# Performance work log

Hardware: AMD Instinct MI355X
Metric: run time of the kernel (lower is better)

The kernel has to match this reference:

```python
import jax, jax.numpy as jnp
import numpy as np

N = 2_000_000
NUM_IN = 9
F1, F2 = 32, 64
NUM_SEG = 100_000
EPS = 1e-5


def setup_inputs() -> dict:
    key = jax.random.key(0)
    ks = jax.random.split(key, 10)
    points = jax.random.normal(ks[0], (N, NUM_IN), dtype=jnp.float32)
    inverse_indices = jax.random.randint(ks[1], (N,), 0, NUM_SEG, dtype=jnp.int64)
    w1 = jax.random.normal(ks[2], (NUM_IN, F1), dtype=jnp.float32) / np.sqrt(NUM_IN)
    b1 = jax.random.normal(ks[3], (F1,), dtype=jnp.float32) * 0.01
    g1 = jnp.ones((F1,), jnp.float32)
    be1 = jnp.zeros((F1,), jnp.float32)
    w2 = jax.random.normal(ks[4], (F1, F2), dtype=jnp.float32) / np.sqrt(F1)
    b2 = jax.random.normal(ks[5], (F2,), dtype=jnp.float32) * 0.01
    g2 = jnp.ones((F2,), jnp.float32)
    be2 = jnp.zeros((F2,), jnp.float32)
    return {
        "points": points, "inverse_indices": inverse_indices, "num_segments": NUM_SEG,
        "w1": w1, "b1": b1, "g1": g1, "be1": be1,
        "w2": w2, "b2": b2, "g2": g2, "be2": be2,
    }


def _linear_bn_relu(x, w, b, gamma, beta):
    # Linear -> BatchNorm1d (training-mode batch stats, biased var, eps=1e-5) -> ReLU
    h = x @ w + b
    mean = h.mean(axis=0)
    var = h.var(axis=0)  # biased, matches torch BN normalization
    h = (h - mean) * jax.lax.rsqrt(var + EPS) * gamma + beta
    return jax.nn.relu(h)


def reference(points, inverse_indices, num_segments, w1, b1, g1, be1, w2, b2, g2, be2):
    feat = _linear_bn_relu(points, w1, b1, g1, be1)
    feat = _linear_bn_relu(feat, w2, b2, g2, be2)
    # scatter_max over dim 0; torch_scatter zero-initializes empty segments,
    # and post-ReLU features are >= 0, so clamp -inf (empty) to 0.
    seg = jax.ops.segment_max(feat, inverse_indices, num_segments=num_segments)
    return jnp.maximum(seg, 0.0)
```

## Files before the change

kernel.cpp:

```cpp
#include <hip/hip_runtime.h>

#define EPS 1e-5f
#define NIN 9
#define F1 32
#define F2 64
#define NMOM 45
#define ROWB 80
#define SHIFT 7
#define NSEGB 128
#define NBMAX 1024
#define BT_BIN 8192
#define WSTRIDE 68
#define NREP 16

#define WS_SC1  192
#define WS_SH1  224
#define WS_W1P  256
#define WS_SC2  544
#define WS_SH2  608

typedef __attribute__((ext_vector_type(8))) short bf16x8;
typedef __attribute__((ext_vector_type(4))) float f32x4;

__device__ __forceinline__ unsigned int f2bf(float f) {
    unsigned int u = __float_as_uint(f);
    return (u + 0x7fffu + ((u >> 16) & 1u)) >> 16;
}
__device__ __forceinline__ unsigned int pack2(float lo, float hi) {
    unsigned int r;
    asm("v_cvt_pk_bf16_f32 %0, %1, %2" : "=v"(r) : "v"(lo), "v"(hi));
    return r;
}

__device__ __forceinline__ void load_pt9(const float* __restrict__ p, float* __restrict__ x)
{
    const float4* p4 = (const float4*)p;
    const float4 a = p4[0];
    const float4 b = p4[1];
    x[0] = a.x; x[1] = a.y; x[2] = a.z; x[3] = a.w;
    x[4] = b.x; x[5] = b.y; x[6] = b.z; x[7] = b.w;
    x[8] = p[8];
}

#define FOR_S(OP) OP(0) OP(1) OP(2) OP(3) OP(4) OP(5) OP(6) OP(7) OP(8)
#define FOR_M(OP) \
    OP(0,0) OP(0,1) OP(0,2) OP(0,3) OP(0,4) OP(0,5) OP(0,6) OP(0,7) OP(0,8) \
    OP(1,1) OP(1,2) OP(1,3) OP(1,4) OP(1,5) OP(1,6) OP(1,7) OP(1,8) \
    OP(2,2) OP(2,3) OP(2,4) OP(2,5) OP(2,6) OP(2,7) OP(2,8) \
    OP(3,3) OP(3,4) OP(3,5) OP(3,6) OP(3,7) OP(3,8) \
    OP(4,4) OP(4,5) OP(4,6) OP(4,7) OP(4,8) \
    OP(5,5) OP(5,6) OP(5,7) OP(5,8) \
    OP(6,6) OP(6,7) OP(6,8) \
    OP(7,7) OP(7,8) \
    OP(8,8)
#define MIDX(k,l) ((k)*NIN - ((k)*((k)-1))/2 + ((l)-(k)))
#define S_DECL(k)   float S_##k = 0.f;
#define M_DECL(k,l) float M_##k##_##l = 0.f;
#define S_ACC(k)    S_##k += x[k];
#define M_ACC(k,l)  M_##k##_##l = fmaf(x[k], x[l], M_##k##_##l);
#define S_RED(k)    S_##k += __shfl_xor(S_##k, off, 64);
#define M_RED(k,l)  M_##k##_##l += __shfl_xor(M_##k##_##l, off, 64);
#define S_ATM(k)    atomicAdd(&red[(k)], S_##k);
#define M_ATM(k,l)  atomicAdd(&red[16 + MIDX(k,l)], M_##k##_##l);

__global__ __launch_bounds__(256, 4) void moments_kernel(
    const float* __restrict__ pts, float* __restrict__ wsrep, int N)
{
    __shared__ float red[64];

    FOR_S(S_DECL)
    FOR_M(M_DECL)

    const int stride = gridDim.x * blockDim.x;
    for (int i = blockIdx.x * blockDim.x + threadIdx.x; i < N; i += stride) {
        float x[NIN];
        load_pt9(pts + (size_t)i * NIN, x);
        FOR_S(S_ACC)
        FOR_M(M_ACC)
    }
#pragma unroll
    for (int off = 32; off > 0; off >>= 1) {
        FOR_S(S_RED)
        FOR_M(M_RED)
    }
    if (threadIdx.x < 64) red[threadIdx.x] = 0.f;
    __syncthreads();
    if ((threadIdx.x & 63) == 0) {
        FOR_S(S_ATM)
        FOR_M(M_ATM)
    }
    __syncthreads();
    if (threadIdx.x < 64)
        atomicAdd(&wsrep[(blockIdx.x & (NREP - 1)) * 64 + threadIdx.x], red[threadIdx.x]);
}

__global__ __launch_bounds__(256) void count_kernel(
    const int* __restrict__ idx, int* __restrict__ histcrep, int N, int nb)
{
    __shared__ int lhist[NBMAX];
    const int tid = threadIdx.x;
    const int t0 = blockIdx.x * BT_BIN;
    for (int t = tid; t < nb; t += 256) lhist[t] = 0;
    __syncthreads();
#pragma unroll 4
    for (int r = 0; r < BT_BIN / 256; ++r) {
        const int i = t0 + r * 256 + tid;
        if (i < N) atomicAdd(&lhist[idx[i] >> SHIFT], 1);
    }
    __syncthreads();
    int* dst = histcrep + (blockIdx.x & (NREP - 1)) * NBMAX;
    for (int t = tid; t < nb; t += 256)
        if (lhist[t] > 0) atomicAdd(&dst[t], lhist[t]);
}

__global__ void scan_coarse_kernel(const int* __restrict__ histcrep,
                                   int* __restrict__ offsets,
                                   int* __restrict__ cursor, int nb)
{
    __shared__ int part[256];
    const int tid = threadIdx.x;
    int v[4];
    int sum = 0;
    const int base = tid * 4;
#pragma unroll
    for (int j = 0; j < 4; ++j) {
        const int i = base + j;
        int a = 0;
        if (i < nb) {
#pragma unroll
            for (int r = 0; r < NREP; ++r) a += histcrep[r * NBMAX + i];
        }
        v[j] = a;
        sum += a;
    }
    part[tid] = sum;
    __syncthreads();
    for (int d = 1; d < 256; d <<= 1) {
        int t = (tid >= d) ? part[tid - d] : 0;
        __syncthreads();
        part[tid] += t;
        __syncthreads();
    }
    int pre = part[tid] - sum;
#pragma unroll
    for (int j = 0; j < 4; ++j) {
        const int i = base + j;
        if (i < nb) { offsets[i] = pre; cursor[i] = pre; }
        pre += v[j];
    }
    if (tid == 255) offsets[nb] = part[255];
}

__global__ void finalize1_kernel(
    const float* __restrict__ w1, const float* __restrict__ b1,
    const float* __restrict__ g1, const float* __restrict__ be1,
    const float* __restrict__ wsrep, float* __restrict__ ws, float invN)
{
    __shared__ float sc1s[F1];
    __shared__ float wsl[64];
    const int j = threadIdx.x;
    if (j < 64) {
        float a = 0.f;
#pragma unroll
        for (int r = 0; r < NREP; ++r) a += wsrep[r * 64 + j];
        wsl[j] = a;
    }
    __syncthreads();
    if (j < F1) {
        float W[NIN];
        float P = 0.f;
#pragma unroll
        for (int k = 0; k < NIN; ++k) {
            W[k] = w1[k * F1 + j];
            P = fmaf(wsl[k], W[k], P);
        }
        float Q = 0.f;
        int m = 0;
#pragma unroll
        for (int k = 0; k < NIN; ++k) {
            Q = fmaf(wsl[16 + m], W[k] * W[k], Q); ++m;
#pragma unroll
            for (int l = k + 1; l < NIN; ++l) {
                Q = fmaf(2.f * wsl[16 + m], W[k] * W[l], Q); ++m;
            }
        }
        const float b = b1[j];
        const float mean = fmaf(P, invN, b);
        const float Eh2 = fmaf(fmaf(2.f * b, P, Q), invN, b * b);
        const float var = Eh2 - mean * mean;
        const float sc = g1[j] * rsqrtf(var + EPS);
        ws[WS_SC1 + j] = sc;
        ws[WS_SH1 + j] = be1[j] - mean * sc;
        sc1s[j] = sc;
    }
    __syncthreads();
    for (int m = threadIdx.x; m < NIN * F1; m += blockDim.x)
        ws[WS_W1P + m] = w1[m] * sc1s[m & (F1 - 1)];
}

__global__ void finalize2_kernel(
    const float* __restrict__ g2, const float* __restrict__ be2,
    const float* __restrict__ b2, const float* __restrict__ ws2rep,
    float* __restrict__ ws, float invN, float padf)
{
    const int j = threadIdx.x;
    if (j < F2) {
        float S = 0.f, SS = 0.f;
#pragma unroll
        for (int r = 0; r < NREP; ++r) {
            S  += ws2rep[r * 128 + j];
            SS += ws2rep[r * 128 + 64 + j];
        }
        const float b = b2[j];
        S  -= padf * b;
        SS -= padf * b * b;
        const float mean = S * invN;
        const float var  = SS * invN - mean * mean;
        const float sc   = g2[j] * rsqrtf(var + EPS);
        ws[WS_SC2 + j] = sc;
        ws[WS_SH2 + j] = be2[j] - mean * sc;
    }
}

__device__ __forceinline__ void f1_row_bf16(
    const float* __restrict__ p, const float* __restrict__ wl,
    const float* __restrict__ sh1, unsigned int* __restrict__ pk )
{
    float x[NIN];
    load_pt9(p, x);
#pragma unroll
    for (int fc = 0; fc < 4; ++fc) {
        float h[8];
#pragma unroll
        for (int jj = 0; jj < 8; ++jj) h[jj] = sh1[fc * 8 + jj];
#pragma unroll
        for (int k = 0; k < NIN; ++k) {
            const float xv = x[k];
#pragma unroll
            for (int jj = 0; jj < 8; ++jj)
                h[jj] = fmaf(xv, wl[k * F1 + fc * 8 + jj], h[jj]);
        }
#pragma unroll
        for (int jj = 0; jj < 4; ++jj)
            pk[fc * 4 + jj] = pack2(fmaxf(h[2 * jj], 0.f), fmaxf(h[2 * jj + 1], 0.f));
    }
}

__global__ __launch_bounds__(256, 3) void f1stats_kernel(
    const float* __restrict__ pts, const float* __restrict__ w2,
    const float* __restrict__ b2, const float* __restrict__ ws,
    float* __restrict__ ws2rep, uint4* __restrict__ f1buf, int N)
{
    __shared__ __align__(16) unsigned char stag[4][64 * ROWB];
    __shared__ float red[2 * F2];

    const int lane = threadIdx.x & 63, wv = threadIdx.x >> 6;
    const int quad = lane >> 4, m16 = lane & 15;

    bf16x8 bfr[4];
#pragma unroll
    for (int nt = 0; nt < 4; ++nt)
#pragma unroll
        for (int j = 0; j < 8; ++j)
            bfr[nt][j] = (short)f2bf(w2[(quad * 8 + j) * F2 + nt * 16 + m16]);
    float b2f[4];
#pragma unroll
    for (int nt = 0; nt < 4; ++nt) b2f[nt] = b2[nt * 16 + m16];

    const float* wl  = ws + WS_W1P;
    const float* sh1 = ws + WS_SH1;
    const f32x4 zero = {0.f, 0.f, 0.f, 0.f};
    float s[4] = {0.f, 0.f, 0.f, 0.f}, ss[4] = {0.f, 0.f, 0.f, 0.f};

    unsigned char* myst = stag[wv];
    const int nchunks = (N + 63) / 64;
    for (int c = blockIdx.x * 4 + wv; c < nchunks; c += gridDim.x * 4) {
        const int i = c * 64 + lane;
        unsigned int pk[16];
        if (i < N) {
            f1_row_bf16(pts + (size_t)i * NIN, wl, sh1, pk);
        } else {
#pragma unroll
            for (int q = 0; q < 16; ++q) pk[q] = 0u;
        }
        uint4* wrow = (uint4*)(myst + lane * ROWB);
#pragma unroll
        for (int cidx = 0; cidx < 4; ++cidx)
            wrow[cidx] = make_uint4(pk[4*cidx+0], pk[4*cidx+1], pk[4*cidx+2], pk[4*cidx+3]);

        if (i < N) {
            uint4* dst = f1buf + (size_t)i * 4;
            dst[0] = make_uint4(pk[0],  pk[1],  pk[2],  pk[3]);
            dst[1] = make_uint4(pk[4],  pk[5],  pk[6],  pk[7]);
            dst[2] = make_uint4(pk[8],  pk[9],  pk[10], pk[11]);
            dst[3] = make_uint4(pk[12], pk[13], pk[14], pk[15]);
        }

        bf16x8 afr[4];
#pragma unroll
        for (int mt = 0; mt < 4; ++mt)
            afr[mt] = *(const bf16x8*)(myst + (mt * 16 + m16) * ROWB + quad * 16);
#pragma unroll
        for (int mt = 0; mt < 4; ++mt) {
#pragma unroll
            for (int nt = 0; nt < 4; ++nt) {
                f32x4 d = __builtin_amdgcn_mfma_f32_16x16x32_bf16(afr[mt], bfr[nt], zero, 0, 0, 0);
#pragma unroll
                for (int rr = 0; rr < 4; ++rr) {
                    const float v = d[rr] + b2f[nt];
                    s[nt] += v;
                    ss[nt] = fmaf(v, v, ss[nt]);
                }
            }
        }
    }

#pragma unroll
    for (int off = 16; off < 64; off <<= 1)
#pragma unroll
        for (int nt = 0; nt < 4; ++nt) {
            s[nt]  += __shfl_xor(s[nt], off, 64);
            ss[nt] += __shfl_xor(ss[nt], off, 64);
        }
    if (threadIdx.x < 2 * F2) red[threadIdx.x] = 0.f;
    __syncthreads();
    if (quad == 0) {
#pragma unroll
        for (int nt = 0; nt < 4; ++nt) {
            atomicAdd(&red[nt * 16 + m16], s[nt]);
            atomicAdd(&red[F2 + nt * 16 + m16], ss[nt]);
        }
    }
    __syncthreads();
    if (threadIdx.x < 2 * F2)
        atomicAdd(&ws2rep[(blockIdx.x & (NREP - 1)) * 128 + threadIdx.x], red[threadIdx.x]);
}

__global__ __launch_bounds__(256) void binning_kernel(
    const int* __restrict__ idx, int* __restrict__ cursor,
    int2* __restrict__ pair, int N, int nb)
{
    __shared__ int lcnt[NBMAX];
    __shared__ int runbase[NBMAX];
    const int tid = threadIdx.x;
    const int t0 = blockIdx.x * BT_BIN;
    for (int t = tid; t < nb; t += 256) lcnt[t] = 0;
    __syncthreads();
#pragma unroll 4
    for (int r = 0; r < BT_BIN / 256; ++r) {
        const int i = t0 + r * 256 + tid;
        if (i < N) atomicAdd(&lcnt[idx[i] >> SHIFT], 1);
    }
    __syncthreads();
    for (int t = tid; t < nb; t += 256) {
        const int c = lcnt[t];
        if (c > 0) runbase[t] = atomicAdd(&cursor[t], c);
        lcnt[t] = 0;
    }
    __syncthreads();
#pragma unroll 4
    for (int r = 0; r < BT_BIN / 256; ++r) {
        const int i = t0 + r * 256 + tid;
        if (i < N) {
            const int sg = idx[i];
            const int bb = sg >> SHIFT;
            const int p = runbase[bb] + atomicAdd(&lcnt[bb], 1);
            pair[p] = make_int2(i, sg);
        }
    }
}

__global__ __launch_bounds__(256, 3) void bucket_scatter_kernel(
    const uint4* __restrict__ f1buf, const int2* __restrict__ pair,
    const float* __restrict__ w2, const float* __restrict__ b2,
    const float* __restrict__ ws, const int* __restrict__ offsets,
    unsigned int* __restrict__ out, int nseg)
{
    __shared__ unsigned int win[NSEGB * WSTRIDE];
    __shared__ int2 prl[4][64];

    const int b = blockIdx.x;
    const int start = offsets[b], end = offsets[b + 1];
    const int tid = threadIdx.x;
    const int lane = tid & 63, wv = tid >> 6;
    const int quad = lane >> 4, m16 = lane & 15;

    for (int t = tid; t < NSEGB * WSTRIDE; t += 256) win[t] = 0u;

    bf16x8 bfr[4];
#pragma unroll
    for (int nt = 0; nt < 4; ++nt)
#pragma unroll
        for (int j = 0; j < 8; ++j)
            bfr[nt][j] = (short)f2bf(w2[(quad * 8 + j) * F2 + nt * 16 + m16]);
    float sc2f[4], shb[4];
#pragma unroll
    for (int nt = 0; nt < 4; ++nt) {
        const int f = nt * 16 + m16;
        sc2f[nt] = ws[WS_SC2 + f];
        shb[nt]  = fmaf(b2[f], sc2f[nt], ws[WS_SH2 + f]);
    }
    const f32x4 zero = {0.f, 0.f, 0.f, 0.f};
    __syncthreads();

    const int segbase = b << SHIFT;
    const int nch = (end - start + 63) >> 6;
    const bf16x8* fb = (const bf16x8*)f1buf;
    for (int c = wv; c < nch; c += 4) {
        const int cbase = start + c * 64;
        const int sp = cbase + lane;
        int2 pr = make_int2(0, -1);
        if (sp < end) {
            pr = pair[sp];
            pr.y -= segbase;
        }
        prl[wv][lane] = pr;

        bf16x8 afr[4];
#pragma unroll
        for (int mt = 0; mt < 4; ++mt) {
            if (cbase + mt * 16 + m16 < end) {
                const int gi = prl[wv][mt * 16 + m16].x;
                afr[mt] = fb[(size_t)gi * 4 + quad];
            } else {
#pragma unroll
                for (int j = 0; j < 8; ++j) afr[mt][j] = 0;
            }
        }
#pragma unroll
        for (int mt = 0; mt < 4; ++mt) {
            f32x4 d[4];
#pragma unroll
            for (int nt = 0; nt < 4; ++nt)
                d[nt] = __builtin_amdgcn_mfma_f32_16x16x32_bf16(afr[mt], bfr[nt], zero, 0, 0, 0);
#pragma unroll
            for (int rr = 0; rr < 4; ++rr) {
                const int sl = prl[wv][mt * 16 + quad * 4 + rr].y;
                if (sl >= 0) {
#pragma unroll
                    for (int nt = 0; nt < 4; ++nt) {
                        const float v = fmaf(d[nt][rr], sc2f[nt], shb[nt]);
                        if (v > 0.f)
                            atomicMax(&win[sl * WSTRIDE + nt * 16 + m16], __float_as_uint(v));
                    }
                }
            }
        }
    }
    __syncthreads();
    const int rows = min(NSEGB, nseg - segbase);
    for (int t = tid; t < rows * 64; t += 256)
        out[(size_t)(segbase + (t >> 6)) * 64 + (t & 63)] = win[(t >> 6) * WSTRIDE + (t & 63)];
}

__global__ __launch_bounds__(256, 3) void stats2_kernel(
    const float* __restrict__ pts, const float* __restrict__ w2,
    const float* __restrict__ b2, const float* __restrict__ ws,
    float* __restrict__ ws2rep, int N)
{
    __shared__ __align__(16) unsigned char stag[4][64 * ROWB];
    __shared__ float red[2 * F2];

    const int lane = threadIdx.x & 63, wv = threadIdx.x >> 6;
    const int quad = lane >> 4, m16 = lane & 15;

    bf16x8 bfr[4];
#pragma unroll
    for (int nt = 0; nt < 4; ++nt)
#pragma unroll
        for (int j = 0; j < 8; ++j)
            bfr[nt][j] = (short)f2bf(w2[(quad * 8 + j) * F2 + nt * 16 + m16]);
    float b2f[4];
#pragma unroll
    for (int nt = 0; nt < 4; ++nt) b2f[nt] = b2[nt * 16 + m16];

    const float* wl  = ws + WS_W1P;
    const float* sh1 = ws + WS_SH1;
    const f32x4 zero = {0.f, 0.f, 0.f, 0.f};
    float s[4] = {0.f, 0.f, 0.f, 0.f}, ss[4] = {0.f, 0.f, 0.f, 0.f};

    unsigned char* myst = stag[wv];
    const int nchunks = (N + 63) / 64;
    for (int c = blockIdx.x * 4 + wv; c < nchunks; c += gridDim.x * 4) {
        const int i = c * 64 + lane;
        unsigned int pk[16];
        if (i < N) {
            f1_row_bf16(pts + (size_t)i * NIN, wl, sh1, pk);
        } else {
#pragma unroll
            for (int q = 0; q < 16; ++q) pk[q] = 0u;
        }
        uint4* wrow = (uint4*)(myst + lane * ROWB);
#pragma unroll
        for (int cidx = 0; cidx < 4; ++cidx)
            wrow[cidx] = make_uint4(pk[4*cidx+0], pk[4*cidx+1], pk[4*cidx+2], pk[4*cidx+3]);

        bf16x8 afr[4];
#pragma unroll
        for (int mt = 0; mt < 4; ++mt)
            afr[mt] = *(const bf16x8*)(myst + (mt * 16 + m16) * ROWB + quad * 16);
#pragma unroll
        for (int mt = 0; mt < 4; ++mt) {
#pragma unroll
            for (int nt = 0; nt < 4; ++nt) {
                f32x4 d = __builtin_amdgcn_mfma_f32_16x16x32_bf16(afr[mt], bfr[nt], zero, 0, 0, 0);
#pragma unroll
                for (int rr = 0; rr < 4; ++rr) {
                    const float v = d[rr] + b2f[nt];
                    s[nt] += v;
                    ss[nt] = fmaf(v, v, ss[nt]);
                }
            }
        }
    }
#pragma unroll
    for (int off = 16; off < 64; off <<= 1)
#pragma unroll
        for (int nt = 0; nt < 4; ++nt) {
            s[nt]  += __shfl_xor(s[nt], off, 64);
            ss[nt] += __shfl_xor(ss[nt], off, 64);
        }
    if (threadIdx.x < 2 * F2) red[threadIdx.x] = 0.f;
    __syncthreads();
    if (quad == 0) {
#pragma unroll
        for (int nt = 0; nt < 4; ++nt) {
            atomicAdd(&red[nt * 16 + m16], s[nt]);
            atomicAdd(&red[F2 + nt * 16 + m16], ss[nt]);
        }
    }
    __syncthreads();
    if (threadIdx.x < 2 * F2)
        atomicAdd(&ws2rep[(blockIdx.x & (NREP - 1)) * 128 + threadIdx.x], red[threadIdx.x]);
}

__global__ __launch_bounds__(256, 2) void bucket_scatter_gather_kernel(
    const float* __restrict__ pts, const int2* __restrict__ pair,
    const float* __restrict__ w2, const float* __restrict__ b2,
    const float* __restrict__ ws, const int* __restrict__ offsets,
    unsigned int* __restrict__ out, int nseg)
{
    __shared__ unsigned int win[NSEGB * WSTRIDE];
    __shared__ __align__(16) unsigned char stag[4][64 * ROWB];
    __shared__ int segl[4][64];

    const int b = blockIdx.x;
    const int start = offsets[b], end = offsets[b + 1];
    const int tid = threadIdx.x;
    const int lane = tid & 63, wv = tid >> 6;
    const int quad = lane >> 4, m16 = lane & 15;

    for (int t = tid; t < NSEGB * WSTRIDE; t += 256) win[t] = 0u;

    bf16x8 bfr[4];
#pragma unroll
    for (int nt = 0; nt < 4; ++nt)
#pragma unroll
        for (int j = 0; j < 8; ++j)
            bfr[nt][j] = (short)f2bf(w2[(quad * 8 + j) * F2 + nt * 16 + m16]);
    float sc2f[4], shb[4];
#pragma unroll
    for (int nt = 0; nt < 4; ++nt) {
        const int f = nt * 16 + m16;
        sc2f[nt] = ws[WS_SC2 + f];
        shb[nt]  = fmaf(b2[f], sc2f[nt], ws[WS_SH2 + f]);
    }
    const float* wl  = ws + WS_W1P;
    const float* sh1 = ws + WS_SH1;
    const f32x4 zero = {0.f, 0.f, 0.f, 0.f};
    __syncthreads();

    const int segbase = b << SHIFT;
    const int nch = (end - start + 63) >> 6;
    unsigned char* myst = stag[wv];
    for (int c = wv; c < nch; c += 4) {
        const int cbase = start + c * 64;
        const int sp = cbase + lane;
        unsigned int pk[16];
        int sl = -1;
        if (sp < end) {
            const int2 pr = pair[sp];
            f1_row_bf16(pts + (size_t)pr.x * NIN, wl, sh1, pk);
            sl = pr.y - segbase;
        } else {
#pragma unroll
            for (int q = 0; q < 16; ++q) pk[q] = 0u;
        }
        segl[wv][lane] = sl;
        uint4* wrow = (uint4*)(myst + lane * ROWB);
#pragma unroll
        for (int cidx = 0; cidx < 4; ++cidx)
            wrow[cidx] = make_uint4(pk[4*cidx+0], pk[4*cidx+1], pk[4*cidx+2], pk[4*cidx+3]);

        bf16x8 afr[4];
#pragma unroll
        for (int mt = 0; mt < 4; ++mt)
            afr[mt] = *(const bf16x8*)(myst + (mt * 16 + m16) * ROWB + quad * 16);
#pragma unroll
        for (int mt = 0; mt < 4; ++mt) {
            f32x4 d[4];
#pragma unroll
            for (int nt = 0; nt < 4; ++nt)
                d[nt] = __builtin_amdgcn_mfma_f32_16x16x32_bf16(afr[mt], bfr[nt], zero, 0, 0, 0);
#pragma unroll
            for (int rr = 0; rr < 4; ++rr) {
                const int sl2 = segl[wv][mt * 16 + quad * 4 + rr];
                if (sl2 >= 0) {
#pragma unroll
                    for (int nt = 0; nt < 4; ++nt) {
                        const float v = fmaf(d[nt][rr], sc2f[nt], shb[nt]);
                        if (v > 0.f)
                            atomicMax(&win[sl2 * WSTRIDE + nt * 16 + m16], __float_as_uint(v));
                    }
                }
            }
        }
    }
    __syncthreads();
    const int rows = min(NSEGB, nseg - segbase);
    for (int t = tid; t < rows * 64; t += 256)
        out[(size_t)(segbase + (t >> 6)) * 64 + (t & 63)] = win[(t >> 6) * WSTRIDE + (t & 63)];
}

extern "C" void kernel_launch(void* const* d_in, const int* in_sizes, int n_in,
                              void* d_out, int out_size, void* d_ws, size_t ws_size,
                              hipStream_t stream)
{
    const float* pts = (const float*)d_in[0];
    const int*   idx = (const int*)d_in[1];
    const float* w1  = (const float*)d_in[3];
    const float* b1  = (const float*)d_in[4];
    const float* g1  = (const float*)d_in[5];
    const float* be1 = (const float*)d_in[6];
    const float* w2  = (const float*)d_in[7];
    const float* b2  = (const float*)d_in[8];
    const float* g2  = (const float*)d_in[9];
    const float* be2 = (const float*)d_in[10];

    const int N = in_sizes[0] / NIN;
    const int nseg = out_size / F2;
    const int nb = (nseg + NSEGB - 1) >> SHIFT;
    const float invN = 1.0f / (float)N;
    const float padf = (float)((64 - (N & 63)) & 63);

    char* base = (char*)d_ws;
    const size_t f1bytes = (size_t)N * 64;
    const size_t pairbytes = (size_t)N * 8;
    const size_t repbytes = (size_t)NREP * NBMAX * 4 + NREP * 64 * 4 + NREP * 128 * 4;
    const size_t tailbytes = 4096 + repbytes + ((size_t)NBMAX + 1 + NBMAX) * sizeof(int) + 256;
    const size_t need_main = f1bytes + pairbytes + tailbytes;

    const int nbin = (N + BT_BIN - 1) / BT_BIN;

    if (ws_size >= need_main) {
        uint4* f1buf    = (uint4*)base;
        int2*  pair     = (int2*)(base + f1bytes);
        char*  tail     = base + f1bytes + pairbytes;
        float* ws       = (float*)tail;
        int*   histcrep = (int*)(tail + 4096);
        float* wsrep    = (float*)(tail + 4096 + (size_t)NREP * NBMAX * 4);
        float* ws2rep   = wsrep + NREP * 64;
        int*   offsets  = (int*)(tail + 4096 + repbytes);
        int*   cursor   = offsets + NBMAX + 1;

        hipMemsetAsync(histcrep, 0, repbytes, stream);

        moments_kernel<<<1024, 256, 0, stream>>>(pts, wsrep, N);
        count_kernel<<<nbin, 256, 0, stream>>>(idx, histcrep, N, nb);
        finalize1_kernel<<<1, 320, 0, stream>>>(w1, b1, g1, be1, wsrep, ws, invN);
        scan_coarse_kernel<<<1, 256, 0, stream>>>(histcrep, offsets, cursor, nb);
        f1stats_kernel<<<1024, 256, 0, stream>>>(pts, w2, b2, ws, ws2rep, f1buf, N);
        binning_kernel<<<nbin, 256, 0, stream>>>(idx, cursor, pair, N, nb);
        finalize2_kernel<<<1, 64, 0, stream>>>(g2, be2, b2, ws2rep, ws, invN, padf);
        bucket_scatter_kernel<<<nb, 256, 0, stream>>>(
            f1buf, pair, w2, b2, ws, offsets, (unsigned int*)d_out, nseg);
    } else {
        int2*  pair     = (int2*)base;
        char*  tail     = base + pairbytes;
        float* ws       = (float*)tail;
        int*   histcrep = (int*)(tail + 4096);
        float* wsrep    = (float*)(tail + 4096 + (size_t)NREP * NBMAX * 4);
        float* ws2rep   = wsrep + NREP * 64;
        int*   offsets  = (int*)(tail + 4096 + repbytes);
        int*   cursor   = offsets + NBMAX + 1;

        hipMemsetAsync(histcrep, 0, repbytes, stream);

        moments_kernel<<<1024, 256, 0, stream>>>(pts, wsrep, N);
        count_kernel<<<nbin, 256, 0, stream>>>(idx, histcrep, N, nb);
        finalize1_kernel<<<1, 320, 0, stream>>>(w1, b1, g1, be1, wsrep, ws, invN);
        scan_coarse_kernel<<<1, 256, 0, stream>>>(histcrep, offsets, cursor, nb);
        binning_kernel<<<nbin, 256, 0, stream>>>(idx, cursor, pair, N, nb);
        stats2_kernel<<<1024, 256, 0, stream>>>(pts, w2, b2, ws, ws2rep, N);
        finalize2_kernel<<<1, 64, 0, stream>>>(g2, be2, b2, ws2rep, ws, invN, padf);
        bucket_scatter_gather_kernel<<<nb, 256, 0, stream>>>(
            pts, pair, w2, b2, ws, offsets, (unsigned int*)d_out, nseg);
    }
}
```

Baseline: 301.9 us.

## Replace atomic cursor binning with per-block rank counting sort and packed pairs

The count pass now records each element's local rank and per-block bucket counts, and a single 1024-thread scan kernel builds per-(bucket,block) bases. This lets the binning pass place elements without re-histogramming and without global atomics. Pairs are packed into one 32-bit word (index<<7 | local segment), which halves pair traffic. The finalize2 kernel is removed and its BN2 statistics are folded into the bucket kernels' prologue. The trade-offs are an extra N*4 rank buffer and a serial per-bucket loop over blocks in the scan. The stats kernel grid and some constants (BT_BIN, NREP) also change.

```diff
diff --git a/kernel.cpp b/kernel.cpp
--- a/kernel.cpp
+++ b/kernel.cpp
@@ -4,20 +4,17 @@
 #define NIN 9
 #define F1 32
 #define F2 64
-#define NMOM 45
 #define ROWB 80
 #define SHIFT 7
 #define NSEGB 128
 #define NBMAX 1024
-#define BT_BIN 8192
+#define BT_BIN 4096
 #define WSTRIDE 68
-#define NREP 16
+#define NREP 32
 
 #define WS_SC1  192
 #define WS_SH1  224
 #define WS_W1P  256
-#define WS_SC2  544
-#define WS_SH2  608
 
 typedef __attribute__((ext_vector_type(8))) short bf16x8;
 typedef __attribute__((ext_vector_type(4))) float f32x4;
@@ -95,7 +92,8 @@
 }
 
 __global__ __launch_bounds__(256) void count_kernel(
-    const int* __restrict__ idx, int* __restrict__ histcrep, int N, int nb)
+    const int* __restrict__ idx, int* __restrict__ rank,
+    int* __restrict__ blkcnt, int N, int nb, int nbin)
 {
     __shared__ int lhist[NBMAX];
     const int tid = threadIdx.x;
@@ -105,50 +103,41 @@
 #pragma unroll 4
     for (int r = 0; r < BT_BIN / 256; ++r) {
         const int i = t0 + r * 256 + tid;
-        if (i < N) atomicAdd(&lhist[idx[i] >> SHIFT], 1);
-    }
-    __syncthreads();
-    int* dst = histcrep + (blockIdx.x & (NREP - 1)) * NBMAX;
+        if (i < N) rank[i] = atomicAdd(&lhist[idx[i] >> SHIFT], 1);
+    }
+    __syncthreads();
     for (int t = tid; t < nb; t += 256)
-        if (lhist[t] > 0) atomicAdd(&dst[t], lhist[t]);
-}
-
-__global__ void scan_coarse_kernel(const int* __restrict__ histcrep,
-                                   int* __restrict__ offsets,
-                                   int* __restrict__ cursor, int nb)
-{
-    __shared__ int part[256];
-    const int tid = threadIdx.x;
-    int v[4];
-    int sum = 0;
-    const int base = tid * 4;
-#pragma unroll
-    for (int j = 0; j < 4; ++j) {
-        const int i = base + j;
-        int a = 0;
-        if (i < nb) {
-#pragma unroll
-            for (int r = 0; r < NREP; ++r) a += histcrep[r * NBMAX + i];
-        }
-        v[j] = a;
-        sum += a;
-    }
-    part[tid] = sum;
-    __syncthreads();
-    for (int d = 1; d < 256; d <<= 1) {
-        int t = (tid >= d) ? part[tid - d] : 0;
+        blkcnt[(size_t)t * nbin + blockIdx.x] = lhist[t];
+}
+
+__global__ void scan_kernel(const int* __restrict__ blkcnt,
+                            int* __restrict__ blkbase,
+                            int* __restrict__ offsets, int nb, int nbin)
+{
+    __shared__ int part[1024];
+    const int t = threadIdx.x;
+    int tot = 0;
+    if (t < nb) {
+        const int* row = blkcnt + (size_t)t * nbin;
+        for (int b = 0; b < nbin; ++b) tot += row[b];
+    }
+    part[t] = tot;
+    __syncthreads();
+    for (int d = 1; d < 1024; d <<= 1) {
+        int v = (t >= d) ? part[t - d] : 0;
         __syncthreads();
-        part[tid] += t;
+        part[t] += v;
         __syncthreads();
     }
-    int pre = part[tid] - sum;
-#pragma unroll
-    for (int j = 0; j < 4; ++j) {
-        const int i = base + j;
-        if (i < nb) { offsets[i] = pre; cursor[i] = pre; }
-        pre += v[j];
-    }
-    if (tid == 255) offsets[nb] = part[255];
+    const int pre = part[t] - tot;
+    if (t < nb) {
+        offsets[t] = pre;
+        int run = pre;
+        const int* row = blkcnt + (size_t)t * nbin;
+        int* brow = blkbase + (size_t)t * nbin;
+        for (int b = 0; b < nbin; ++b) { brow[b] = run; run += row[b]; }
+    }
+    if (t == 1023) offsets[nb] = part[1023];
 }
 
 __global__ void finalize1_kernel(
@@ -198,30 +187,6 @@
         ws[WS_W1P + m] = w1[m] * sc1s[m & (F1 - 1)];
 }
 
-__global__ void finalize2_kernel(
-    const float* __restrict__ g2, const float* __restrict__ be2,
-    const float* __restrict__ b2, const float* __restrict__ ws2rep,
-    float* __restrict__ ws, float invN, float padf)
-{
-    const int j = threadIdx.x;
-    if (j < F2) {
-        float S = 0.f, SS = 0.f;
-#pragma unroll
-        for (int r = 0; r < NREP; ++r) {
-            S  += ws2rep[r * 128 + j];
-            SS += ws2rep[r * 128 + 64 + j];
-        }
-        const float b = b2[j];
-        S  -= padf * b;
-        SS -= padf * b * b;
-        const float mean = S * invN;
-        const float var  = SS * invN - mean * mean;
-        const float sc   = g2[j] * rsqrtf(var + EPS);
-        ws[WS_SC2 + j] = sc;
-        ws[WS_SH2 + j] = be2[j] - mean * sc;
-    }
-}
-
 __device__ __forceinline__ void f1_row_bf16(
     const float* __restrict__ p, const float* __restrict__ wl,
     const float* __restrict__ sh1, unsigned int* __restrict__ pk )
@@ -337,47 +302,36 @@
 }
 
 __global__ __launch_bounds__(256) void binning_kernel(
-    const int* __restrict__ idx, int* __restrict__ cursor,
-    int2* __restrict__ pair, int N, int nb)
-{
-    __shared__ int lcnt[NBMAX];
+    const int* __restrict__ idx, const int* __restrict__ rank,
+    const int* __restrict__ blkbase, unsigned int* __restrict__ pairpk,
+    int N, int nb, int nbin)
+{
     __shared__ int runbase[NBMAX];
     const int tid = threadIdx.x;
-    const int t0 = blockIdx.x * BT_BIN;
-    for (int t = tid; t < nb; t += 256) lcnt[t] = 0;
-    __syncthreads();
-#pragma unroll 4
-    for (int r = 0; r < BT_BIN / 256; ++r) {
-        const int i = t0 + r * 256 + tid;
-        if (i < N) atomicAdd(&lcnt[idx[i] >> SHIFT], 1);
-    }
-    __syncthreads();
-    for (int t = tid; t < nb; t += 256) {
-        const int c = lcnt[t];
-        if (c > 0) runbase[t] = atomicAdd(&cursor[t], c);
-        lcnt[t] = 0;
-    }
+    const int b = blockIdx.x;
+    const int t0 = b * BT_BIN;
+    for (int t = tid; t < nb; t += 256) runbase[t] = blkbase[(size_t)t * nbin + b];
     __syncthreads();
 #pragma unroll 4
     for (int r = 0; r < BT_BIN / 256; ++r) {
         const int i = t0 + r * 256 + tid;
         if (i < N) {
             const int sg = idx[i];
-            const int bb = sg >> SHIFT;
-            const int p = runbase[bb] + atomicAdd(&lcnt[bb], 1);
-            pair[p] = make_int2(i, sg);
+            const int p = runbase[sg >> SHIFT] + rank[i];
+            pairpk[p] = ((unsigned)i << SHIFT) | (unsigned)(sg & (NSEGB - 1));
         }
     }
 }
 
 __global__ __launch_bounds__(256, 3) void bucket_scatter_kernel(
-    const uint4* __restrict__ f1buf, const int2* __restrict__ pair,
+    const uint4* __restrict__ f1buf, const unsigned int* __restrict__ pairpk,
     const float* __restrict__ w2, const float* __restrict__ b2,
-    const float* __restrict__ ws, const int* __restrict__ offsets,
-    unsigned int* __restrict__ out, int nseg)
+    const float* __restrict__ g2, const float* __restrict__ be2,
+    const float* __restrict__ ws2rep, const int* __restrict__ offsets,
+    unsigned int* __restrict__ out, int nseg, float invN, float padf)
 {
     __shared__ unsigned int win[NSEGB * WSTRIDE];
-    __shared__ int2 prl[4][64];
+    __shared__ int prl[4][64];
 
     const int b = blockIdx.x;
     const int start = offsets[b], end = offsets[b + 1];
@@ -397,30 +351,38 @@
 #pragma unroll
     for (int nt = 0; nt < 4; ++nt) {
         const int f = nt * 16 + m16;
-        sc2f[nt] = ws[WS_SC2 + f];
-        shb[nt]  = fmaf(b2[f], sc2f[nt], ws[WS_SH2 + f]);
+        float S = 0.f, SS = 0.f;
+#pragma unroll
+        for (int r = 0; r < NREP; ++r) {
+            S  += ws2rep[r * 128 + f];
+            SS += ws2rep[r * 128 + 64 + f];
+        }
+        const float bb2 = b2[f];
+        S  -= padf * bb2;
+        SS -= padf * bb2 * bb2;
+        const float mean = S * invN;
+        const float var  = SS * invN - mean * mean;
+        const float sc   = g2[f] * rsqrtf(var + EPS);
+        sc2f[nt] = sc;
+        shb[nt]  = fmaf(bb2, sc, be2[f] - mean * sc);
     }
     const f32x4 zero = {0.f, 0.f, 0.f, 0.f};
     __syncthreads();
 
-    const int segbase = b << SHIFT;
     const int nch = (end - start + 63) >> 6;
     const bf16x8* fb = (const bf16x8*)f1buf;
     for (int c = wv; c < nch; c += 4) {
         const int cbase = start + c * 64;
         const int sp = cbase + lane;
-        int2 pr = make_int2(0, -1);
-        if (sp < end) {
-            pr = pair[sp];
-            pr.y -= segbase;
-        }
+        int pr = -1;
+        if (sp < end) pr = (int)pairpk[sp];
         prl[wv][lane] = pr;
 
         bf16x8 afr[4];
 #pragma unroll
         for (int mt = 0; mt < 4; ++mt) {
             if (cbase + mt * 16 + m16 < end) {
-                const int gi = prl[wv][mt * 16 + m16].x;
+                const unsigned int gi = ((unsigned int)prl[wv][mt * 16 + m16]) >> SHIFT;
                 afr[mt] = fb[(size_t)gi * 4 + quad];
             } else {
 #pragma unroll
@@ -435,19 +397,21 @@
                 d[nt] = __builtin_amdgcn_mfma_f32_16x16x32_bf16(afr[mt], bfr[nt], zero, 0, 0, 0);
 #pragma unroll
             for (int rr = 0; rr < 4; ++rr) {
-                const int sl = prl[wv][mt * 16 + quad * 4 + rr].y;
-                if (sl >= 0) {
+                const int v = prl[wv][mt * 16 + quad * 4 + rr];
+                if (v >= 0) {
+                    const int sl = v & (NSEGB - 1);
 #pragma unroll
                     for (int nt = 0; nt < 4; ++nt) {
-                        const float v = fmaf(d[nt][rr], sc2f[nt], shb[nt]);
-                        if (v > 0.f)
-                            atomicMax(&win[sl * WSTRIDE + nt * 16 + m16], __float_as_uint(v));
+                        const float vv = fmaf(d[nt][rr], sc2f[nt], shb[nt]);
+                        if (vv > 0.f)
+                            atomicMax(&win[sl * WSTRIDE + nt * 16 + m16], __float_as_uint(vv));
                     }
                 }
             }
         }
     }
     __syncthreads();
+    const int segbase = b << SHIFT;
     const int rows = min(NSEGB, nseg - segbase);
     for (int t = tid; t < rows * 64; t += 256)
         out[(size_t)(segbase + (t >> 6)) * 64 + (t & 63)] = win[(t >> 6) * WSTRIDE + (t & 63)];
@@ -535,10 +499,12 @@
 }
 
 __global__ __launch_bounds__(256, 2) void bucket_scatter_gather_kernel(
-    const float* __restrict__ pts, const int2* __restrict__ pair,
+    const float* __restrict__ pts, const unsigned int* __restrict__ pairpk,
     const float* __restrict__ w2, const float* __restrict__ b2,
-    const float* __restrict__ ws, const int* __restrict__ offsets,
-    unsigned int* __restrict__ out, int nseg)
+    const float* __restrict__ g2, const float* __restrict__ be2,
+    const float* __restrict__ ws, const float* __restrict__ ws2rep,
+    const int* __restrict__ offsets,
+    unsigned int* __restrict__ out, int nseg, float invN, float padf)
 {
     __shared__ unsigned int win[NSEGB * WSTRIDE];
     __shared__ __align__(16) unsigned char stag[4][64 * ROWB];
@@ -562,15 +528,26 @@
 #pragma unroll
     for (int nt = 0; nt < 4; ++nt) {
         const int f = nt * 16 + m16;
-        sc2f[nt] = ws[WS_SC2 + f];
-        shb[nt]  = fmaf(b2[f], sc2f[nt], ws[WS_SH2 + f]);
+        float S = 0.f, SS = 0.f;
+#pragma unroll
+        for (int r = 0; r < NREP; ++r) {
+            S  += ws2rep[r * 128 + f];
+            SS += ws2rep[r * 128 + 64 + f];
+        }
+        const float bb2 = b2[f];
+        S  -= padf * bb2;
+        SS -= padf * bb2 * bb2;
+        const float mean = S * invN;
+        const float var  = SS * invN - mean * mean;
+        const float sc   = g2[f] * rsqrtf(var + EPS);
+        sc2f[nt] = sc;
+        shb[nt]  = fmaf(bb2, sc, be2[f] - mean * sc);
     }
     const float* wl  = ws + WS_W1P;
     const float* sh1 = ws + WS_SH1;
     const f32x4 zero = {0.f, 0.f, 0.f, 0.f};
     __syncthreads();
 
-    const int segbase = b << SHIFT;
     const int nch = (end - start + 63) >> 6;
     unsigned char* myst = stag[wv];
     for (int c = wv; c < nch; c += 4) {
@@ -579,9 +556,9 @@
         unsigned int pk[16];
         int sl = -1;
         if (sp < end) {
-            const int2 pr = pair[sp];
-            f1_row_bf16(pts + (size_t)pr.x * NIN, wl, sh1, pk);
-            sl = pr.y - segbase;
+            const unsigned int v = pairpk[sp];
+            f1_row_bf16(pts + (size_t)(v >> SHIFT) * NIN, wl, sh1, pk);
+            sl = (int)(v & (NSEGB - 1));
         } else {
 #pragma unroll
             for (int q = 0; q < 16; ++q) pk[q] = 0u;
@@ -608,15 +585,16 @@
                 if (sl2 >= 0) {
 #pragma unroll
                     for (int nt = 0; nt < 4; ++nt) {
-                        const float v = fmaf(d[nt][rr], sc2f[nt], shb[nt]);
-                        if (v > 0.f)
-                            atomicMax(&win[sl2 * WSTRIDE + nt * 16 + m16], __float_as_uint(v));
+                        const float vv = fmaf(d[nt][rr], sc2f[nt], shb[nt]);
+                        if (vv > 0.f)
+                            atomicMax(&win[sl2 * WSTRIDE + nt * 16 + m16], __float_as_uint(vv));
                     }
                 }
             }
         }
     }
     __syncthreads();
+    const int segbase = b << SHIFT;
     const int rows = min(NSEGB, nseg - segbase);
     for (int t = tid; t < rows * 64; t += 256)
         out[(size_t)(segbase + (t >> 6)) * 64 + (t & 63)] = win[(t >> 6) * WSTRIDE + (t & 63)];
@@ -639,61 +617,65 @@
 
     const int N = in_sizes[0] / NIN;
     const int nseg = out_size / F2;
-    const int nb = (nseg + NSEGB - 1) >> SHIFT;
+    int nb = (nseg + NSEGB - 1) >> SHIFT;
+    if (nb > NBMAX) nb = NBMAX;
+    const int nbin = (N + BT_BIN - 1) / BT_BIN;
     const float invN = 1.0f / (float)N;
     const float padf = (float)((64 - (N & 63)) & 63);
 
     char* base = (char*)d_ws;
-    const size_t f1bytes = (size_t)N * 64;
-    const size_t pairbytes = (size_t)N * 8;
-    const size_t repbytes = (size_t)NREP * NBMAX * 4 + NREP * 64 * 4 + NREP * 128 * 4;
-    const size_t tailbytes = 4096 + repbytes + ((size_t)NBMAX + 1 + NBMAX) * sizeof(int) + 256;
-    const size_t need_main = f1bytes + pairbytes + tailbytes;
-
-    const int nbin = (N + BT_BIN - 1) / BT_BIN;
+    const size_t f1bytes   = (size_t)N * 64;
+    const size_t pairbytes = (size_t)N * 4;
+    const size_t rankbytes = (size_t)N * 4;
+    const size_t repbytes  = (size_t)NREP * 192 * 4;
+    const size_t blkbytes  = (size_t)nb * nbin * 4;
+    const size_t tailbytes = 4096 + repbytes + 2 * blkbytes + ((size_t)NBMAX + 1) * 4 + 256;
+    const size_t need_main = f1bytes + pairbytes + rankbytes + tailbytes;
 
     if (ws_size >= need_main) {
-        uint4* f1buf    = (uint4*)base;
-        int2*  pair     = (int2*)(base + f1bytes);
-        char*  tail     = base + f1bytes + pairbytes;
-        float* ws       = (float*)tail;
-        int*   histcrep = (int*)(tail + 4096);
-        float* wsrep    = (float*)(tail + 4096 + (size_t)NREP * NBMAX * 4);
-        float* ws2rep   = wsrep + NREP * 64;
-        int*   offsets  = (int*)(tail + 4096 + repbytes);
-        int*   cursor   = offsets + NBMAX + 1;
-
-        hipMemsetAsync(histcrep, 0, repbytes, stream);
+        uint4*        f1buf   = (uint4*)base;
+        unsigned int* pairpk  = (unsigned int*)(base + f1bytes);
+        int*          rank    = (int*)(base + f1bytes + pairbytes);
+        char*         tail    = base + f1bytes + pairbytes + rankbytes;
+        float*        ws      = (float*)tail;
+        float*        wsrep   = (float*)(tail + 4096);
+        float*        ws2rep  = wsrep + NREP * 64;
+        int*          blkcnt  = (int*)(tail + 4096 + repbytes);
+        int*          blkbase = (int*)(tail + 4096 + repbytes + blkbytes);
+        int*          offsets = (int*)(tail + 4096 + repbytes + 2 * blkbytes);
+
+        hipMemsetAsync(wsrep, 0, repbytes, stream);
 
         moments_kernel<<<1024, 256, 0, stream>>>(pts, wsrep, N);
-        count_kernel<<<nbin, 256, 0, stream>>>(idx, histcrep, N, nb);
+        count_kernel<<<nbin, 256, 0, stream>>>(idx, rank, blkcnt, N, nb, nbin);
         finalize1_kernel<<<1, 320, 0, stream>>>(w1, b1, g1, be1, wsrep, ws, invN);
-        scan_coarse_kernel<<<1, 256, 0, stream>>>(histcrep, offsets, cursor, nb);
-        f1stats_kernel<<<1024, 256, 0, stream>>>(pts, w2, b2, ws, ws2rep, f1buf, N);
-        binning_kernel<<<nbin, 256, 0, stream>>>(idx, cursor, pair, N, nb);
-        finalize2_kernel<<<1, 64, 0, stream>>>(g2, be2, b2, ws2rep, ws, invN, padf);
+        scan_kernel<<<1, 1024, 0, stream>>>(blkcnt, blkbase, offsets, nb, nbin);
+        f1stats_kernel<<<1792, 256, 0, stream>>>(pts, w2, b2, ws, ws2rep, f1buf, N);
+        binning_kernel<<<nbin, 256, 0, stream>>>(idx, rank, blkbase, pairpk, N, nb, nbin);
         bucket_scatter_kernel<<<nb, 256, 0, stream>>>(
-            f1buf, pair, w2, b2, ws, offsets, (unsigned int*)d_out, nseg);
+            f1buf, pairpk, w2, b2, g2, be2, ws2rep, offsets,
+            (unsigned int*)d_out, nseg, invN, padf);
     } else {
-        int2*  pair     = (int2*)base;
-        char*  tail     = base + pairbytes;
-        float* ws       = (float*)tail;
-        int*   histcrep = (int*)(tail + 4096);
-        float* wsrep    = (float*)(tail + 4096 + (size_t)NREP * NBMAX * 4);
-        float* ws2rep   = wsrep + NREP * 64;
-        int*   offsets  = (int*)(tail + 4096 + repbytes);
-        int*   cursor   = offsets + NBMAX + 1;
-
-        hipMemsetAsync(histcrep, 0, repbytes, stream);
+        unsigned int* pairpk  = (unsigned int*)base;
+        int*          rank    = (int*)(base + pairbytes);
+        char*         tail    = base + pairbytes + rankbytes;
+        float*        ws      = (float*)tail;
+        float*        wsrep   = (float*)(tail + 4096);
+        float*        ws2rep  = wsrep + NREP * 64;
+        int*          blkcnt  = (int*)(tail + 4096 + repbytes);
+        int*          blkbase = (int*)(tail + 4096 + repbytes + blkbytes);
+        int*          offsets = (int*)(tail + 4096 + repbytes + 2 * blkbytes);
+
+        hipMemsetAsync(wsrep, 0, repbytes, stream);
 
         moments_kernel<<<1024, 256, 0, stream>>>(pts, wsrep, N);
-        count_kernel<<<nbin, 256, 0, stream>>>(idx, histcrep, N, nb);
+        count_kernel<<<nbin, 256, 0, stream>>>(idx, rank, blkcnt, N, nb, nbin);
         finalize1_kernel<<<1, 320, 0, stream>>>(w1, b1, g1, be1, wsrep, ws, invN);
-        scan_coarse_kernel<<<1, 256, 0, stream>>>(histcrep, offsets, cursor, nb);
-        binning_kernel<<<nbin, 256, 0, stream>>>(idx, cursor, pair, N, nb);
+        scan_kernel<<<1, 1024, 0, stream>>>(blkcnt, blkbase, offsets, nb, nbin);
+        binning_kernel<<<nbin, 256, 0, stream>>>(idx, rank, blkbase, pairpk, N, nb, nbin);
         stats2_kernel<<<1024, 256, 0, stream>>>(pts, w2, b2, ws, ws2rep, N);
-        finalize2_kernel<<<1, 64, 0, stream>>>(g2, be2, b2, ws2rep, ws, invN, padf);
         bucket_scatter_gather_kernel<<<nb, 256, 0, stream>>>(
-            pts, pair, w2, b2, ws, offsets, (unsigned int*)d_out, nseg);
-    }
-}
+            pts, pairpk, w2, b2, g2, be2, ws, ws2rep, offsets,
+            (unsigned int*)d_out, nseg, invN, padf);
+    }
+}
```

Result: slower. 946.4 us (+213.5%).
